# Performance work log

Hardware: AMD Instinct MI355X
Metric: run time of the kernel (lower is better)

## Reference

```python
import jax, jax.numpy as jnp
import numpy as np

N = 1_000_000   # total nodes
F = 128         # num_node_features
P = 16          # num_graph_coordinators
G = 128         # graphs in batch


def setup_inputs() -> dict:
    key = jax.random.key(0)
    k_x, k_p, k_b = jax.random.split(key, 3)
    learnable_param = jax.random.normal(k_p, (P, F), dtype=jnp.float32)
    # last_updated_param is a deepcopy of learnable_param at init time
    last_updated_param = learnable_param
    x = jax.random.normal(k_x, (N, F), dtype=jnp.float32)
    # seed exact copies of coordinator params into x so matches occur
    # (mirrors add_learnable_features_with_no_grad appending coordinator rows)
    seed_idx = jnp.arange(P) * (N // P)  # P well-separated rows
    x = x.at[seed_idx].set(last_updated_param)
    batch = jnp.sort(jax.random.randint(k_b, (N,), 0, G)).astype(jnp.int64)
    return {"x": x, "batch": batch,
            "learnable_param": learnable_param,
            "last_updated_param": last_updated_param}


def reference(x, batch, learnable_param, last_updated_param):
    # For every node row, check exact equality against each last_updated_param
    # the enumerate loop where each match overwrites the row). Comparisons run
    # against the running (already-replaced) x, matching the in-place torch
    # semantics. batch/graph grouping does not affect the result: every node is
    # visited exactly once regardless of loop order.
    def body(x_cur, pair):
        last_p, learn_p = pair  # [F], [F]
        m = jnp.all(x_cur == last_p[None, :], axis=1)  # [N] exact row match
        x_new = jnp.where(m[:, None], learn_p[None, :], x_cur)
        return x_new, None

    x_out, _ = jax.lax.scan(body, x, (last_updated_param, learnable_param))
    return x_out
```

## Files before the change

### kernel.cpp

```cpp
#include <hip/hip_runtime.h>


#define F_DIM 128
#define P_DIM 16
#define UNROLL 4

typedef float f32x4 __attribute__((ext_vector_type(4)));

__global__ __launch_bounds__(256) void copy_fix_kernel(
    const float* __restrict__ x,
    const float* __restrict__ learn,
    const float* __restrict__ last,
    float* __restrict__ out,
    int n_rows)
{
    float sig[P_DIM];
    #pragma unroll
    for (int p = 0; p < P_DIM; ++p) sig[p] = last[p * F_DIM];

    const f32x4* __restrict__ src = reinterpret_cast<const f32x4*>(x);
    f32x4*       __restrict__ dst = reinterpret_cast<f32x4*>(out);

    const int tid  = threadIdx.x;
    const int half = (tid >> 5) & 1;
    const int sl   = tid & 31;

    const int total4  = n_rows * (F_DIM / 4);
    const int chunk   = 256 * UNROLL;
    const int gstride = chunk * gridDim.x;
    const int total4_full = total4 & ~(chunk - 1);

    int base = blockIdx.x * chunk;
    for (; base < total4_full; base += gstride) {
        const int i0 = base + tid;

        f32x4 v[UNROLL];
        #pragma unroll
        for (int m = 0; m < UNROLL; ++m)
            v[m] = __builtin_nontemporal_load(&src[i0 + m * 256]);

        #pragma unroll
        for (int m = 0; m < UNROLL; ++m) {
            bool hit = false;
            if (sl == 0) {
                #pragma unroll
                for (int p = 0; p < P_DIM; ++p) hit |= (v[m].x == sig[p]);
            }
            if (__any(hit)) {
                for (int p = 0; p < P_DIM; ++p) {
                    const f32x4 lp =
                        *reinterpret_cast<const f32x4*>(&last[p * F_DIM + sl * 4]);
                    const bool eq = (v[m].x == lp.x) & (v[m].y == lp.y) &
                                    (v[m].z == lp.z) & (v[m].w == lp.w);
                    const unsigned long long bm = __ballot(eq);
                    const unsigned int mh = (unsigned int)(bm >> (half * 32));
                    if (mh == 0xFFFFFFFFu)
                        v[m] = *reinterpret_cast<const f32x4*>(
                                   &learn[p * F_DIM + sl * 4]);
                }
            }
        }

        #pragma unroll
        for (int m = 0; m < UNROLL; ++m)
            __builtin_nontemporal_store(v[m], &dst[i0 + m * 256]);
    }

    for (; base < total4; base += gstride) {
        const int i0 = base + tid;
        #pragma unroll
        for (int m = 0; m < UNROLL; ++m) {
            const int i4 = i0 + m * 256;
            if (i4 >= total4) continue;
            f32x4 v = __builtin_nontemporal_load(&src[i4]);
            bool hit = false;
            if (sl == 0) {
                #pragma unroll
                for (int p = 0; p < P_DIM; ++p) hit |= (v.x == sig[p]);
            }
            if (__any(hit)) {
                for (int p = 0; p < P_DIM; ++p) {
                    const f32x4 lp =
                        *reinterpret_cast<const f32x4*>(&last[p * F_DIM + sl * 4]);
                    const bool eq = (v.x == lp.x) & (v.y == lp.y) &
                                    (v.z == lp.z) & (v.w == lp.w);
                    const unsigned long long bm = __ballot(eq);
                    const unsigned int mh = (unsigned int)(bm >> (half * 32));
                    if (mh == 0xFFFFFFFFu)
                        v = *reinterpret_cast<const f32x4*>(
                                &learn[p * F_DIM + sl * 4]);
                }
            }
            __builtin_nontemporal_store(v, &dst[i4]);
        }
    }
}

extern "C" void kernel_launch(void* const* d_in, const int* in_sizes, int n_in,
                              void* d_out, int out_size, void* d_ws, size_t ws_size,
                              hipStream_t stream) {
    const float* x     = (const float*)d_in[0];
    const float* learn = (const float*)d_in[2];
    const float* last  = (const float*)d_in[3];
    float*       out   = (float*)d_out;

    const int n_rows = in_sizes[0] / F_DIM;

    copy_fix_kernel<<<2048, 256, 0, stream>>>(x, learn, last, out, n_rows);
}
```

Baseline: 182.4 us.

## Use one-shot grid, wider unroll, and shuffle-based signature prefilter

Replaces the grid-stride loop with one block per chunk sized to the input and doubles the per-thread unroll to 8 vectors. The 16-way serial signature check on lane 0 becomes a cross-lane broadcast: each lane compares the row's first element against one of the 16 parameter signatures, then a wave-wide vote decides. Loads switch from nontemporal to regular loads while stores stay nontemporal. This is meant to cut per-wave ALU in the prefilter and raise memory-level parallelism, at the cost of more registers and a much larger launch.

```diff
diff --git a/kernel.cpp b/kernel.cpp
--- a/kernel.cpp
+++ b/kernel.cpp
@@ -3,7 +3,8 @@
 
 #define F_DIM 128
 #define P_DIM 16
-#define UNROLL 4
+#define UNROLL 8
+#define CHUNK (256 * UNROLL)
 
 typedef float f32x4 __attribute__((ext_vector_type(4)));
 
@@ -12,41 +13,31 @@
     const float* __restrict__ learn,
     const float* __restrict__ last,
     float* __restrict__ out,
-    int n_rows)
+    int total4)
 {
-    float sig[P_DIM];
-    #pragma unroll
-    for (int p = 0; p < P_DIM; ++p) sig[p] = last[p * F_DIM];
+    const int tid  = threadIdx.x;
+    const int half = (tid >> 5) & 1;
+    const int sl   = tid & 31;
+
+    const float mysig = last[(tid & 15) * F_DIM];
 
     const f32x4* __restrict__ src = reinterpret_cast<const f32x4*>(x);
     f32x4*       __restrict__ dst = reinterpret_cast<f32x4*>(out);
 
-    const int tid  = threadIdx.x;
-    const int half = (tid >> 5) & 1;
-    const int sl   = tid & 31;
+    const int base = blockIdx.x * CHUNK;
 
-    const int total4  = n_rows * (F_DIM / 4);
-    const int chunk   = 256 * UNROLL;
-    const int gstride = chunk * gridDim.x;
-    const int total4_full = total4 & ~(chunk - 1);
-
-    int base = blockIdx.x * chunk;
-    for (; base < total4_full; base += gstride) {
+    if (base + CHUNK <= total4) {
         const int i0 = base + tid;
 
         f32x4 v[UNROLL];
         #pragma unroll
         for (int m = 0; m < UNROLL; ++m)
-            v[m] = __builtin_nontemporal_load(&src[i0 + m * 256]);
+            v[m] = src[i0 + m * 256];
 
         #pragma unroll
         for (int m = 0; m < UNROLL; ++m) {
-            bool hit = false;
-            if (sl == 0) {
-                #pragma unroll
-                for (int p = 0; p < P_DIM; ++p) hit |= (v[m].x == sig[p]);
-            }
-            if (__any(hit)) {
+            const float bv = __shfl(v[m].x, tid & 32);
+            if (__any(bv == mysig)) {
                 for (int p = 0; p < P_DIM; ++p) {
                     const f32x4 lp =
                         *reinterpret_cast<const f32x4*>(&last[p * F_DIM + sl * 4]);
@@ -64,21 +55,14 @@
         #pragma unroll
         for (int m = 0; m < UNROLL; ++m)
             __builtin_nontemporal_store(v[m], &dst[i0 + m * 256]);
-    }
-
-    for (; base < total4; base += gstride) {
-        const int i0 = base + tid;
+    } else {
         #pragma unroll
         for (int m = 0; m < UNROLL; ++m) {
-            const int i4 = i0 + m * 256;
+            const int i4 = base + tid + m * 256;
             if (i4 >= total4) continue;
-            f32x4 v = __builtin_nontemporal_load(&src[i4]);
-            bool hit = false;
-            if (sl == 0) {
-                #pragma unroll
-                for (int p = 0; p < P_DIM; ++p) hit |= (v.x == sig[p]);
-            }
-            if (__any(hit)) {
+            f32x4 v = src[i4];
+            const float bv = __shfl(v.x, tid & 32);
+            if (__any(bv == mysig)) {
                 for (int p = 0; p < P_DIM; ++p) {
                     const f32x4 lp =
                         *reinterpret_cast<const f32x4*>(&last[p * F_DIM + sl * 4]);
@@ -105,6 +89,8 @@
     float*       out   = (float*)d_out;
 
     const int n_rows = in_sizes[0] / F_DIM;
+    const int total4 = n_rows * (F_DIM / 4);
+    const int grid   = (total4 + CHUNK - 1) / CHUNK;
 
-    copy_fix_kernel<<<2048, 256, 0, stream>>>(x, learn, last, out, n_rows);
+    copy_fix_kernel<<<grid, 256, 0, stream>>>(x, learn, last, out, total4);
 }
```

Result: no change. 185.8 us (+1.8%).
